# Kernel optimization log

Measured on AMD Instinct MI355X. Metric: run time of the kernel, lower is better.

## Reference

```python
import jax, jax.numpy as jnp
import numpy as np

N_ATOMS = 5000
N_PAIRS = 160000
N_STRUCT = 16
N_SPECIES = 4
L_MAX = 2
K = 128            # k_max per l (rectangular)
N_BASIS = 8        # radial basis size
RAD_HIDDEN = 32    # radial MLP hidden
CUTOFF = 5.0
MSG_SCALE = 0.1767767   # ~1/sqrt(avg_degree)
INIT_SCALE = 0.2        # hypers['initial_scaling']


def _orthogonal(key, n):
    m = jax.random.normal(key, (n, n))
    q, r = jnp.linalg.qr(m)
    return q * jnp.sign(jnp.diag(r))[None, :]


def setup_inputs() -> dict:
    key = jax.random.key(0)
    ks = jax.random.split(key, 24)
    positions = jax.random.normal(ks[0], (N_ATOMS, 3)) * 1.5
    cells = jax.random.normal(ks[1], (N_STRUCT, 3, 3)) * 0.5
    species = jax.random.randint(ks[2], (N_ATOMS,), 0, N_SPECIES)
    cell_shifts = jax.random.randint(ks[3], (N_PAIRS, 3), 0, 3).astype(jnp.int32)
    center_indices = jax.random.randint(ks[4], (N_PAIRS,), 0, N_ATOMS)
    neighbor_indices = jax.random.randint(ks[5], (N_PAIRS,), 0, N_ATOMS)
    structure_pairs = jax.random.randint(ks[6], (N_PAIRS,), 0, N_STRUCT)
    s = lambda k, sh, f: jax.random.normal(k, sh) * f
    params = dict(
        embed=s(ks[7], (N_SPECIES, K), 1.0),
        rad_w1=s(ks[8], (N_BASIS, RAD_HIDDEN), 0.3), rad_b1=jnp.zeros((RAD_HIDDEN,)),
        rad_w2=s(ks[9], (RAD_HIDDEN, (L_MAX + 1) * K), 0.3), rad_b2=jnp.zeros(((L_MAX + 1) * K,)),
        erad_w1=s(ks[10], (N_BASIS, RAD_HIDDEN), 0.3), erad_b1=jnp.zeros((RAD_HIDDEN,)),
        erad_w2=s(ks[11], (RAD_HIDDEN, (L_MAX + 1) * K), 0.3), erad_b2=jnp.zeros(((L_MAX + 1) * K,)),
        mix_a=s(ks[12], (L_MAX + 1, K), 0.5),
        emix_a=s(ks[13], (L_MAX + 1, K), 0.5),
        head_w1=s(ks[14], (K, K), 0.1), head_b1=jnp.zeros((K,)),
        head_w2=s(ks[15], (K, K), 0.1), head_b2=jnp.zeros((K,)),
        last_w=s(ks[16], (K, 1), 0.1), last_b=jnp.zeros((1,)),
        U2=_orthogonal(ks[20], 9),  # orthogonal CG change-of-basis, U @ U.T = I
    )
    return dict(positions=positions, cells=cells, species=species,
                cell_shifts=cell_shifts, center_indices=center_indices,
                neighbor_indices=neighbor_indices, structure_pairs=structure_pairs,
                **params)


def _sph(unit):
    # real spherical harmonics up to l=2, inputs are unit vectors [P,3]
    x, y, z = unit[:, 0], unit[:, 1], unit[:, 2]
    sh0 = jnp.ones_like(x)[:, None]
    sh1 = jnp.stack([y, z, x], axis=1)
    c = jnp.sqrt(3.0)
    sh2 = jnp.stack([c * x * y, c * y * z, 0.5 * (3 * z * z - 1.0),
                     c * x * z, 0.5 * c * (x * x - y * y)], axis=1)
    return [sh0, sh1, sh2]


def _radial(d, w1, b1, w2, b2):
    # Gaussian radial basis * smooth cutoff -> MLP -> per-l K channels
    centers = jnp.linspace(0.0, CUTOFF, N_BASIS)
    rb = jnp.exp(-((d[:, None] - centers[None, :]) ** 2) / (2.0 * 0.5 ** 2))
    fcut = jnp.where(d < CUTOFF, 0.5 * (jnp.cos(jnp.pi * d / CUTOFF) + 1.0), 0.0)
    h = jax.nn.silu((rb * fcut[:, None]) @ w1 + b1)
    return (h @ w2 + b2).reshape(-1, L_MAX + 1, K)  # [P, l, K]


def _uncouple(f, l, U2):
    # coupled [N, 2l+1, K] -> uncoupled matrix [N, 3, 3, K] (padded_l = 2)
    if l == 0:
        return f[:, :, None, :]
    n, _, k = f.shape
    vec = jnp.zeros((n, 9, k), f.dtype)
    off = 1 if l == 1 else 4
    vec = vec.at[:, off:off + 2 * l + 1, :].set(f)
    unc = jnp.einsum('qp,nqk->npk', U2, vec)  # U2.T @ vec
    return unc.reshape(n, 3, 3, k)


def _couple(unc, l, U2):
    if l == 0:
        return unc[:, :, 0, :]
    n, k = unc.shape[0], unc.shape[-1]
    vec = jnp.einsum('pq,nqk->npk', U2, unc.reshape(n, 9, k))
    off = 1 if l == 1 else 4
    return vec[:, off:off + 2 * l + 1, :]


def _cg_iterate(feats, U2, mix):
    # CG tensor product iteration in the uncoupled (matrix) basis:
    # matrix product A@A is equivariant under A -> D A D^T
    out = []
    for l, f in enumerate(feats):
        A = _uncouple(f, l, U2)
        C = jnp.einsum('nimk,nmjk->nijk', A, A)
        out.append(_couple(A + C * mix[l][None, None, None, :], l, U2))
    return out


def _forward(positions, cells, embed, rad_w1, rad_b1, rad_w2, rad_b2,
             erad_w1, erad_b1, erad_w2, erad_b2, mix_a, emix_a,
             head_w1, head_b1, head_w2, head_b2, last_w, last_b, U2,
             species, cell_shifts, center_indices, neighbor_indices, structure_pairs):
    # pair vectors with PBC shifts
    shifts = cell_shifts.astype(positions.dtype) - 1.0  # -> {-1,0,1}
    vec = positions[neighbor_indices] - positions[center_indices] \
        + jnp.einsum('pi,pij->pj', shifts, cells[structure_pairs])
    d = jnp.sqrt(jnp.sum(vec * vec, axis=1) + 1e-12)
    unit = vec / d[:, None]
    sh = [s * INIT_SCALE for s in _sph(unit)]
    Rk = _radial(d, rad_w1, rad_b1, rad_w2, rad_b2)      # [P, 3, K]
    emb_n = embed[species][neighbor_indices]             # [P, K]

    # invariant message passing: sh_l x radial x neighbor embedding, scatter to centers
    feats = []
    for l in range(L_MAX + 1):
        msg = sh[l][:, :, None] * Rk[:, l, None, :] * emb_n[:, None, :]
        feats.append(jax.ops.segment_sum(msg, center_indices, num_segments=N_ATOMS) * MSG_SCALE)

    feats = _cg_iterate(feats, U2, mix_a)

    # equivariant message passing layer
    Rke = _radial(d, erad_w1, erad_b1, erad_w2, erad_b2)
    inv_n = feats[0][neighbor_indices, 0, :]             # [P, K] invariant part
    new = []
    for l in range(L_MAX + 1):
        g = feats[l][neighbor_indices]                   # [P, 2l+1, K]
        msg = sh[l][:, :, None] * Rke[:, l, None, :] * inv_n[:, None, :] \
            + Rke[:, 0, None, :] * g
        new.append(feats[l] + jax.ops.segment_sum(msg, center_indices, num_segments=N_ATOMS) * MSG_SCALE)

    feats = _cg_iterate(new, U2, emix_a)

    # scalar (l=0) MLP head + last linear layer
    h = feats[0][:, 0, :]
    h = jax.nn.silu(h @ head_w1 + head_b1)
    h = jax.nn.silu(h @ head_w2 + head_b2)
    return h @ last_w + last_b  # [N_ATOMS, 1]


def reference(positions, cells, species, cell_shifts, center_indices,
              neighbor_indices, structure_pairs, embed, rad_w1, rad_b1, rad_w2,
              rad_b2, erad_w1, erad_b1, erad_w2, erad_b2, mix_a, emix_a,
              head_w1, head_b1, head_w2, head_b2, last_w, last_b, U2):
    return _forward(positions, cells, embed, rad_w1, rad_b1, rad_w2, rad_b2,
                    erad_w1, erad_b1, erad_w2, erad_b2, mix_a, emix_a,
                    head_w1, head_b1, head_w2, head_b2, last_w, last_b, U2,
                    species, cell_shifts, center_indices, neighbor_indices,
                    structure_pairs)
```

## Files before the change

kernel.cpp:

```cpp
#include <hip/hip_runtime.h>

constexpr int   kAtoms  = 5000;
constexpr int   kPairs  = 160000;
constexpr int   KD      = 128;
constexpr int   NB      = 8;
constexpr int   RH      = 32;
constexpr float kCutoff = 5.0f;
constexpr float kPi     = 3.14159265358979323846f;
constexpr float C1 = 0.2f * 0.1767767f;
constexpr float C2 = 1.2f * 0.1767767f;
constexpr int   CHUNK = 96;

__device__ __forceinline__ float silu(float x) { return x / (1.0f + __expf(-x)); }


__global__ __launch_bounds__(256) void hist_kernel(
    const int* __restrict__ ctr, int* __restrict__ cnt)
{
    int p = blockIdx.x * 256 + threadIdx.x;
    atomicAdd(cnt + ctr[p], 1);
}

__global__ __launch_bounds__(1024) void scan_kernel(
    const int* __restrict__ cnt, int* __restrict__ off, int* __restrict__ cur)
{
    __shared__ int s_part[1024];
    const int CH = 5;
    int t = threadIdx.x;
    int base = t * CH;
    int loc[CH];
    int run = 0;
    #pragma unroll
    for (int i = 0; i < CH; i++) {
        int idx = base + i;
        int v = (idx < kAtoms) ? cnt[idx] : 0;
        loc[i] = run;
        run += v;
    }
    s_part[t] = run;
    __syncthreads();
    for (int st = 1; st < 1024; st <<= 1) {
        int v = (t >= st) ? s_part[t - st] : 0;
        __syncthreads();
        s_part[t] += v;
        __syncthreads();
    }
    int excl = (t > 0) ? s_part[t - 1] : 0;
    #pragma unroll
    for (int i = 0; i < CH; i++) {
        int idx = base + i;
        if (idx < kAtoms) { off[idx] = excl + loc[i]; cur[idx] = excl + loc[i]; }
    }
    if (t == 1023) off[kAtoms] = s_part[1023];
}

__global__ __launch_bounds__(256) void build_kernel(
    const float* __restrict__ pos, const float* __restrict__ cells,
    const int* __restrict__ species, const int* __restrict__ shifts,
    const int* __restrict__ ctr, const int* __restrict__ nbr,
    const int* __restrict__ spair,
    int* __restrict__ cur, int* __restrict__ nbrs_s, int* __restrict__ specs_s,
    float* __restrict__ rbf_s)
{
    int p = blockIdx.x * 256 + threadIdx.x;
    int ci = ctr[p], ni = nbr[p], sp = spair[p];
    float s0 = (float)shifts[p * 3 + 0] - 1.0f;
    float s1 = (float)shifts[p * 3 + 1] - 1.0f;
    float s2 = (float)shifts[p * 3 + 2] - 1.0f;
    const float* C = cells + sp * 9;
    float vx = pos[ni * 3 + 0] - pos[ci * 3 + 0] + s0 * C[0] + s1 * C[3] + s2 * C[6];
    float vy = pos[ni * 3 + 1] - pos[ci * 3 + 1] + s0 * C[1] + s1 * C[4] + s2 * C[7];
    float vz = pos[ni * 3 + 2] - pos[ci * 3 + 2] + s0 * C[2] + s1 * C[5] + s2 * C[8];
    float d = sqrtf(vx * vx + vy * vy + vz * vz + 1e-12f);
    float fcut = (d < kCutoff) ? 0.5f * (__cosf(kPi * d / kCutoff) + 1.0f) : 0.0f;

    int slot = atomicAdd(cur + ci, 1);
    nbrs_s[slot]  = ni;
    specs_s[slot] = species[ni];

    float r[NB];
    #pragma unroll
    for (int i = 0; i < NB; i++) {
        float tt = d - (kCutoff / (NB - 1)) * (float)i;
        r[i] = __expf(-2.0f * tt * tt) * fcut;
    }
    float4* dst = (float4*)(rbf_s + (size_t)slot * NB);
    dst[0] = make_float4(r[0], r[1], r[2], r[3]);
    dst[1] = make_float4(r[4], r[5], r[6], r[7]);
}

__global__ __launch_bounds__(64) void f0_kernel(
    const float* __restrict__ rbf_s, const int* __restrict__ specs_s,
    const int* __restrict__ off,
    const float* __restrict__ embed,
    const float* __restrict__ w1, const float* __restrict__ b1,
    const float* __restrict__ w2, const float* __restrict__ b2,
    const float* __restrict__ mix,
    float* __restrict__ G0)
{
    __shared__ float s_w1[NB][RH];
    __shared__ float s_b1v[RH];
    __shared__ float s_Hp[2][4][RH];
    __shared__ float s_H[4][RH];
    __shared__ float s_np[2][4];
    __shared__ float s_nc[4];

    int t = threadIdx.x;
    for (int idx = t; idx < NB * RH; idx += 64)
        s_w1[idx >> 5][idx & 31] = w1[idx];
    if (t < RH) s_b1v[t] = b1[t];
    __syncthreads();

    int a = blockIdx.x;
    int start = off[a], m = off[a + 1] - start;

    int g = t >> 5, j = t & 31;
    float H0 = 0, H1 = 0, H2 = 0, H3 = 0;
    int   n0 = 0, n1 = 0, n2 = 0, n3 = 0;
    float b1j = s_b1v[j];
    for (int pr = g; pr < m; pr += 2) {
        const float* rb = rbf_s + (size_t)(start + pr) * NB;
        float acc = b1j;
        #pragma unroll
        for (int i = 0; i < NB; i++) acc += rb[i] * s_w1[i][j];
        float h = silu(acc);
        int s = specs_s[start + pr];
        H0 += (s == 0) ? h : 0.0f;  H1 += (s == 1) ? h : 0.0f;
        H2 += (s == 2) ? h : 0.0f;  H3 += (s == 3) ? h : 0.0f;
        n0 += (s == 0); n1 += (s == 1); n2 += (s == 2); n3 += (s == 3);
    }
    s_Hp[g][0][j] = H0; s_Hp[g][1][j] = H1;
    s_Hp[g][2][j] = H2; s_Hp[g][3][j] = H3;
    if (j == 0) {
        s_np[g][0] = (float)n0; s_np[g][1] = (float)n1;
        s_np[g][2] = (float)n2; s_np[g][3] = (float)n3;
    }
    __syncthreads();
    for (int e = t; e < 4 * RH; e += 64) {
        int s = e >> 5, jj = e & 31;
        s_H[s][jj] = s_Hp[0][s][jj] + s_Hp[1][s][jj];
    }
    if (t < 4) s_nc[t] = s_np[0][t] + s_np[1][t];
    __syncthreads();

    float nc0 = s_nc[0], nc1 = s_nc[1], nc2 = s_nc[2], nc3 = s_nc[3];
    #pragma unroll
    for (int half = 0; half < 2; half++) {
        int k = t + 64 * half;
        float e0 = embed[0 * KD + k], e1 = embed[1 * KD + k];
        float e2 = embed[2 * KD + k], e3 = embed[3 * KD + k];
        float P0 = 0, P1 = 0, P2 = 0, P3 = 0;
        #pragma unroll 2
        for (int jq = 0; jq < RH / 4; jq++) {
            float4 h0 = *(const float4*)&s_H[0][4 * jq];
            float4 h1 = *(const float4*)&s_H[1][4 * jq];
            float4 h2 = *(const float4*)&s_H[2][4 * jq];
            float4 h3 = *(const float4*)&s_H[3][4 * jq];
            float wa = w2[(4 * jq + 0) * (3 * KD) + k];
            float wb = w2[(4 * jq + 1) * (3 * KD) + k];
            float wc = w2[(4 * jq + 2) * (3 * KD) + k];
            float wd = w2[(4 * jq + 3) * (3 * KD) + k];
            P0 += h0.x * wa + h0.y * wb + h0.z * wc + h0.w * wd;
            P1 += h1.x * wa + h1.y * wb + h1.z * wc + h1.w * wd;
            P2 += h2.x * wa + h2.y * wb + h2.z * wc + h2.w * wd;
            P3 += h3.x * wa + h3.y * wb + h3.z * wc + h3.w * wd;
        }
        float F = b2[k] * (nc0 * e0 + nc1 * e1 + nc2 * e2 + nc3 * e3)
                + e0 * P0 + e1 * P1 + e2 * P2 + e3 * P3;
        float F0v = C1 * F;
        G0[(size_t)a * KD + k] = F0v + F0v * F0v * mix[k];
    }
}

__global__ __launch_bounds__(64) void d0_kernel(
    const float* __restrict__ rbf_s, const int* __restrict__ nbrs_s,
    const int* __restrict__ off,
    const float* __restrict__ w1, const float* __restrict__ b1,
    const float* __restrict__ w2, const float* __restrict__ b2,
    const float* __restrict__ emix,
    const float* __restrict__ G0,
    float* __restrict__ V)
{
    __shared__ float s_w1[NB][RH];
    __shared__ float s_b1v[RH];
    __shared__ float s_h[CHUNK][RH];
    __shared__ int   s_nbr[CHUNK];

    int t = threadIdx.x;
    for (int idx = t; idx < NB * RH; idx += 64)
        s_w1[idx >> 5][idx & 31] = w1[idx];
    if (t < RH) s_b1v[t] = b1[t];

    int a = blockIdx.x;
    int start = off[a], end = off[a + 1];
    int k0 = t, k1 = t + 64;

    float w2c0[RH], w2c1[RH];
    #pragma unroll
    for (int j = 0; j < RH; j++) {
        w2c0[j] = w2[j * (3 * KD) + k0];
        w2c1[j] = w2[j * (3 * KD) + k1];
    }
    float b2k0 = b2[k0], b2k1 = b2[k1];

    int g = t >> 5, j = t & 31;
    float b1j = s_b1v[j];

    float Dacc0 = 0.0f, Dacc1 = 0.0f;
    for (int c = start; c < end; c += CHUNK) {
        int m = min(CHUNK, end - c);
        __syncthreads();
        for (int pr = g; pr < m; pr += 2) {
            const float* rb = rbf_s + (size_t)(c + pr) * NB;
            float acc = b1j;
            #pragma unroll
            for (int i = 0; i < NB; i++) acc += rb[i] * s_w1[i][j];
            s_h[pr][j] = silu(acc);
        }
        for (int i = t; i < m; i += 64) s_nbr[i] = nbrs_s[c + i];
        __syncthreads();
        for (int i = 0; i < m; i++) {
            const float* gbase = G0 + (size_t)s_nbr[i] * KD;
            float gv0 = gbase[k0];
            float gv1 = gbase[k1];
            float R0 = b2k0, R1 = b2k1;
            #pragma unroll
            for (int jq = 0; jq < RH / 4; jq++) {
                float4 h4 = *(const float4*)&s_h[i][4 * jq];
                R0 += h4.x * w2c0[4 * jq + 0] + h4.y * w2c0[4 * jq + 1]
                    + h4.z * w2c0[4 * jq + 2] + h4.w * w2c0[4 * jq + 3];
                R1 += h4.x * w2c1[4 * jq + 0] + h4.y * w2c1[4 * jq + 1]
                    + h4.z * w2c1[4 * jq + 2] + h4.w * w2c1[4 * jq + 3];
            }
            Dacc0 += R0 * gv0;
            Dacc1 += R1 * gv1;
        }
    }
    float n0 = G0[(size_t)a * KD + k0] + C2 * Dacc0;
    float n1 = G0[(size_t)a * KD + k1] + C2 * Dacc1;
    V[(size_t)a * KD + k0] = n0 + n0 * n0 * emix[k0];
    V[(size_t)a * KD + k1] = n1 + n1 * n1 * emix[k1];
}

__global__ __launch_bounds__(128) void head_kernel(
    const float* __restrict__ V,
    const float* __restrict__ w1, const float* __restrict__ b1,
    const float* __restrict__ w2, const float* __restrict__ b2,
    const float* __restrict__ lw, const float* __restrict__ lb,
    float* __restrict__ out)
{
    __shared__ float s_a[8][KD];
    __shared__ float s_b[8][KD];
    int j = threadIdx.x;
    int abase = blockIdx.x * 8;

    #pragma unroll
    for (int a = 0; a < 8; a++) {
        int ga = abase + a;
        s_a[a][j] = (ga < kAtoms) ? V[(size_t)ga * KD + j] : 0.0f;
    }
    __syncthreads();

    float acc[8];
    float bj = b1[j];
    #pragma unroll
    for (int a = 0; a < 8; a++) acc[a] = bj;
    for (int kk = 0; kk < KD; kk += 4) {
        float wa = w1[(kk + 0) * KD + j], wb = w1[(kk + 1) * KD + j];
        float wc = w1[(kk + 2) * KD + j], wd = w1[(kk + 3) * KD + j];
        #pragma unroll
        for (int a = 0; a < 8; a++) {
            float4 v = *(const float4*)&s_a[a][kk];
            acc[a] += v.x * wa + v.y * wb + v.z * wc + v.w * wd;
        }
    }
    #pragma unroll
    for (int a = 0; a < 8; a++) s_b[a][j] = silu(acc[a]);
    __syncthreads();

    float b2j = b2[j];
    #pragma unroll
    for (int a = 0; a < 8; a++) acc[a] = b2j;
    for (int kk = 0; kk < KD; kk += 4) {
        float wa = w2[(kk + 0) * KD + j], wb = w2[(kk + 1) * KD + j];
        float wc = w2[(kk + 2) * KD + j], wd = w2[(kk + 3) * KD + j];
        #pragma unroll
        for (int a = 0; a < 8; a++) {
            float4 v = *(const float4*)&s_b[a][kk];
            acc[a] += v.x * wa + v.y * wb + v.z * wc + v.w * wd;
        }
    }
    float lwj = lw[j];
    __syncthreads();
    #pragma unroll
    for (int a = 0; a < 8; a++) s_a[a][j] = silu(acc[a]) * lwj;
    __syncthreads();
    for (int s = 64; s > 0; s >>= 1) {
        if (j < s) {
            #pragma unroll
            for (int a = 0; a < 8; a++) s_a[a][j] += s_a[a][j + s];
        }
        __syncthreads();
    }
    if (j < 8) {
        int ga = abase + j;
        if (ga < kAtoms) out[ga] = s_a[j][0] + lb[0];
    }
}

extern "C" void kernel_launch(void* const* d_in, const int* in_sizes, int n_in,
                              void* d_out, int out_size, void* d_ws, size_t ws_size,
                              hipStream_t stream) {
    const float* positions = (const float*)d_in[0];
    const float* cells     = (const float*)d_in[1];
    const int*   species   = (const int*)d_in[2];
    const int*   shifts    = (const int*)d_in[3];
    const int*   ctr       = (const int*)d_in[4];
    const int*   nbr       = (const int*)d_in[5];
    const int*   spair     = (const int*)d_in[6];
    const float* embed     = (const float*)d_in[7];
    const float* rad_w1    = (const float*)d_in[8];
    const float* rad_b1    = (const float*)d_in[9];
    const float* rad_w2    = (const float*)d_in[10];
    const float* rad_b2    = (const float*)d_in[11];
    const float* erad_w1   = (const float*)d_in[12];
    const float* erad_b1   = (const float*)d_in[13];
    const float* erad_w2   = (const float*)d_in[14];
    const float* erad_b2   = (const float*)d_in[15];
    const float* mix_a     = (const float*)d_in[16];
    const float* emix_a    = (const float*)d_in[17];
    const float* head_w1   = (const float*)d_in[18];
    const float* head_b1   = (const float*)d_in[19];
    const float* head_w2   = (const float*)d_in[20];
    const float* head_b2   = (const float*)d_in[21];
    const float* last_w    = (const float*)d_in[22];
    const float* last_b    = (const float*)d_in[23];

    float* rbf_s = (float*)d_ws;
    float* G0    = rbf_s + (size_t)kPairs * NB;
    float* V     = G0    + (size_t)kAtoms * KD;
    int*   cnt   = (int*)(V + (size_t)kAtoms * KD);
    int*   off   = cnt + kAtoms;
    int*   cur   = off + kAtoms + 1;
    int*   nbrs  = cur + kAtoms;
    int*   specs = nbrs + kPairs;

    hipMemsetAsync(cnt, 0, kAtoms * sizeof(int), stream);

    hist_kernel<<<kPairs / 256, 256, 0, stream>>>(ctr, cnt);
    scan_kernel<<<1, 1024, 0, stream>>>(cnt, off, cur);
    build_kernel<<<kPairs / 256, 256, 0, stream>>>(
        positions, cells, species, shifts, ctr, nbr, spair,
        cur, nbrs, specs, rbf_s);

    f0_kernel<<<kAtoms, 64, 0, stream>>>(
        rbf_s, specs, off, embed, rad_w1, rad_b1, rad_w2, rad_b2,
        mix_a, G0);

    d0_kernel<<<kAtoms, 64, 0, stream>>>(
        rbf_s, nbrs, off, erad_w1, erad_b1, erad_w2, erad_b2,
        emix_a, G0, V);

    head_kernel<<<(kAtoms + 7) / 8, 128, 0, stream>>>(
        V, head_w1, head_b1, head_w2, head_b2, last_w, last_b,
        (float*)d_out);
}
```

Before: 222.1 us.

## Pack four atoms per block with wave-local barriers in f0 and d0 kernels

The f0 and d0 kernels now run 256-thread blocks with one 64-lane wave per atom, so four atoms share a block. Their per-atom shared buffers become per-wave, and block-wide __syncthreads inside the per-atom loops become wave barriers. The d0 chunk size drops from 96 to 32 pairs so each wave's shared staging stays small. The aim is to amortise weight loading and cut block-scheduling and barrier overhead, at the cost of relying on wave-synchronous execution for correctness.

```diff
diff --git a/kernel.cpp b/kernel.cpp
--- a/kernel.cpp
+++ b/kernel.cpp
@@ -9,9 +9,10 @@
 constexpr float kPi     = 3.14159265358979323846f;
 constexpr float C1 = 0.2f * 0.1767767f;
 constexpr float C2 = 1.2f * 0.1767767f;
-constexpr int   CHUNK = 96;
+constexpr int   WCH = 32;
 
 __device__ __forceinline__ float silu(float x) { return x / (1.0f + __expf(-x)); }
+__device__ __forceinline__ void wave_fence() { __builtin_amdgcn_wave_barrier(); }
 
 
 __global__ __launch_bounds__(256) void hist_kernel(
@@ -89,7 +90,7 @@
     dst[1] = make_float4(r[4], r[5], r[6], r[7]);
 }
 
-__global__ __launch_bounds__(64) void f0_kernel(
+__global__ __launch_bounds__(256) void f0_kernel(
     const float* __restrict__ rbf_s, const int* __restrict__ specs_s,
     const int* __restrict__ off,
     const float* __restrict__ embed,
@@ -100,21 +101,20 @@
 {
     __shared__ float s_w1[NB][RH];
     __shared__ float s_b1v[RH];
-    __shared__ float s_Hp[2][4][RH];
-    __shared__ float s_H[4][RH];
-    __shared__ float s_np[2][4];
-    __shared__ float s_nc[4];
-
-    int t = threadIdx.x;
-    for (int idx = t; idx < NB * RH; idx += 64)
+    __shared__ float s_H[4][2][4][RH];
+    __shared__ float s_Hc[4][4][RH];
+    __shared__ float s_n[4][2][4];
+
+    int t = threadIdx.x, w = t >> 6, lane = t & 63;
+    for (int idx = t; idx < NB * RH; idx += 256)
         s_w1[idx >> 5][idx & 31] = w1[idx];
     if (t < RH) s_b1v[t] = b1[t];
     __syncthreads();
 
-    int a = blockIdx.x;
+    int a = blockIdx.x * 4 + w;
     int start = off[a], m = off[a + 1] - start;
 
-    int g = t >> 5, j = t & 31;
+    int g = lane >> 5, j = lane & 31;
     float H0 = 0, H1 = 0, H2 = 0, H3 = 0;
     int   n0 = 0, n1 = 0, n2 = 0, n3 = 0;
     float b1j = s_b1v[j];
@@ -129,33 +129,36 @@
         H2 += (s == 2) ? h : 0.0f;  H3 += (s == 3) ? h : 0.0f;
         n0 += (s == 0); n1 += (s == 1); n2 += (s == 2); n3 += (s == 3);
     }
-    s_Hp[g][0][j] = H0; s_Hp[g][1][j] = H1;
-    s_Hp[g][2][j] = H2; s_Hp[g][3][j] = H3;
+    s_H[w][g][0][j] = H0; s_H[w][g][1][j] = H1;
+    s_H[w][g][2][j] = H2; s_H[w][g][3][j] = H3;
     if (j == 0) {
-        s_np[g][0] = (float)n0; s_np[g][1] = (float)n1;
-        s_np[g][2] = (float)n2; s_np[g][3] = (float)n3;
-    }
-    __syncthreads();
-    for (int e = t; e < 4 * RH; e += 64) {
+        s_n[w][g][0] = (float)n0; s_n[w][g][1] = (float)n1;
+        s_n[w][g][2] = (float)n2; s_n[w][g][3] = (float)n3;
+    }
+    wave_fence();
+    #pragma unroll
+    for (int e = lane; e < 4 * RH; e += 64) {
         int s = e >> 5, jj = e & 31;
-        s_H[s][jj] = s_Hp[0][s][jj] + s_Hp[1][s][jj];
-    }
-    if (t < 4) s_nc[t] = s_np[0][t] + s_np[1][t];
-    __syncthreads();
-
-    float nc0 = s_nc[0], nc1 = s_nc[1], nc2 = s_nc[2], nc3 = s_nc[3];
+        s_Hc[w][s][jj] = s_H[w][0][s][jj] + s_H[w][1][s][jj];
+    }
+    wave_fence();
+    float nc0 = s_n[w][0][0] + s_n[w][1][0];
+    float nc1 = s_n[w][0][1] + s_n[w][1][1];
+    float nc2 = s_n[w][0][2] + s_n[w][1][2];
+    float nc3 = s_n[w][0][3] + s_n[w][1][3];
+
     #pragma unroll
     for (int half = 0; half < 2; half++) {
-        int k = t + 64 * half;
+        int k = lane + 64 * half;
         float e0 = embed[0 * KD + k], e1 = embed[1 * KD + k];
         float e2 = embed[2 * KD + k], e3 = embed[3 * KD + k];
         float P0 = 0, P1 = 0, P2 = 0, P3 = 0;
-        #pragma unroll 2
+        #pragma unroll
         for (int jq = 0; jq < RH / 4; jq++) {
-            float4 h0 = *(const float4*)&s_H[0][4 * jq];
-            float4 h1 = *(const float4*)&s_H[1][4 * jq];
-            float4 h2 = *(const float4*)&s_H[2][4 * jq];
-            float4 h3 = *(const float4*)&s_H[3][4 * jq];
+            float4 h0 = *(const float4*)&s_Hc[w][0][4 * jq];
+            float4 h1 = *(const float4*)&s_Hc[w][1][4 * jq];
+            float4 h2 = *(const float4*)&s_Hc[w][2][4 * jq];
+            float4 h3 = *(const float4*)&s_Hc[w][3][4 * jq];
             float wa = w2[(4 * jq + 0) * (3 * KD) + k];
             float wb = w2[(4 * jq + 1) * (3 * KD) + k];
             float wc = w2[(4 * jq + 2) * (3 * KD) + k];
@@ -172,7 +175,7 @@
     }
 }
 
-__global__ __launch_bounds__(64) void d0_kernel(
+__global__ __launch_bounds__(256) void d0_kernel(
     const float* __restrict__ rbf_s, const int* __restrict__ nbrs_s,
     const int* __restrict__ off,
     const float* __restrict__ w1, const float* __restrict__ b1,
@@ -183,17 +186,18 @@
 {
     __shared__ float s_w1[NB][RH];
     __shared__ float s_b1v[RH];
-    __shared__ float s_h[CHUNK][RH];
-    __shared__ int   s_nbr[CHUNK];
-
-    int t = threadIdx.x;
-    for (int idx = t; idx < NB * RH; idx += 64)
+    __shared__ float s_h[4][WCH][RH];
+    __shared__ int   s_nbr[4][WCH];
+
+    int t = threadIdx.x, w = t >> 6, lane = t & 63;
+    for (int idx = t; idx < NB * RH; idx += 256)
         s_w1[idx >> 5][idx & 31] = w1[idx];
     if (t < RH) s_b1v[t] = b1[t];
-
-    int a = blockIdx.x;
+    __syncthreads();
+
+    int a = blockIdx.x * 4 + w;
     int start = off[a], end = off[a + 1];
-    int k0 = t, k1 = t + 64;
+    int k0 = lane, k1 = lane + 64;
 
     float w2c0[RH], w2c1[RH];
     #pragma unroll
@@ -203,30 +207,31 @@
     }
     float b2k0 = b2[k0], b2k1 = b2[k1];
 
-    int g = t >> 5, j = t & 31;
+    int g = lane >> 5, j = lane & 31;
     float b1j = s_b1v[j];
 
     float Dacc0 = 0.0f, Dacc1 = 0.0f;
-    for (int c = start; c < end; c += CHUNK) {
-        int m = min(CHUNK, end - c);
-        __syncthreads();
+    for (int c = start; c < end; c += WCH) {
+        int m = min(WCH, end - c);
+        wave_fence();
         for (int pr = g; pr < m; pr += 2) {
             const float* rb = rbf_s + (size_t)(c + pr) * NB;
             float acc = b1j;
             #pragma unroll
             for (int i = 0; i < NB; i++) acc += rb[i] * s_w1[i][j];
-            s_h[pr][j] = silu(acc);
-        }
-        for (int i = t; i < m; i += 64) s_nbr[i] = nbrs_s[c + i];
-        __syncthreads();
+            s_h[w][pr][j] = silu(acc);
+        }
+        if (lane < m) s_nbr[w][lane] = nbrs_s[c + lane];
+        wave_fence();
+        #pragma unroll 2
         for (int i = 0; i < m; i++) {
-            const float* gbase = G0 + (size_t)s_nbr[i] * KD;
+            const float* gbase = G0 + (size_t)s_nbr[w][i] * KD;
             float gv0 = gbase[k0];
             float gv1 = gbase[k1];
             float R0 = b2k0, R1 = b2k1;
             #pragma unroll
             for (int jq = 0; jq < RH / 4; jq++) {
-                float4 h4 = *(const float4*)&s_h[i][4 * jq];
+                float4 h4 = *(const float4*)&s_h[w][i][4 * jq];
                 R0 += h4.x * w2c0[4 * jq + 0] + h4.y * w2c0[4 * jq + 1]
                     + h4.z * w2c0[4 * jq + 2] + h4.w * w2c0[4 * jq + 3];
                 R1 += h4.x * w2c1[4 * jq + 0] + h4.y * w2c1[4 * jq + 1]
@@ -353,11 +358,11 @@
         positions, cells, species, shifts, ctr, nbr, spair,
         cur, nbrs, specs, rbf_s);
 
-    f0_kernel<<<kAtoms, 64, 0, stream>>>(
+    f0_kernel<<<kAtoms / 4, 256, 0, stream>>>(
         rbf_s, specs, off, embed, rad_w1, rad_b1, rad_w2, rad_b2,
         mix_a, G0);
 
-    d0_kernel<<<kAtoms, 64, 0, stream>>>(
+    d0_kernel<<<kAtoms / 4, 256, 0, stream>>>(
         rbf_s, nbrs, off, erad_w1, erad_b1, erad_w2, erad_b2,
         emix_a, G0, V);
 
```

Result: no change. 225.4 us (+1.5%).
